# Optimization experiments

Measured on AMD Instinct MI355X. Metric: run time of the kernel, lower is better.

## Reference

```python
import jax, jax.numpy as jnp
import numpy as np

B, N, DIM, HEAD = 4, 2048, 1024, 16
HD = DIM // HEAD
LN_EPS = 1e-5


def setup_inputs() -> dict:
    key = jax.random.key(0)
    k1, k2, k3, k4 = jax.random.split(key, 4)
    x = jax.random.normal(k1, (B, N, DIM), dtype=jnp.float32)
    A = jax.random.normal(k2, (B, N, HEAD, 1), dtype=jnp.float32)
    ln_w = jnp.ones((DIM,), dtype=jnp.float32)
    ln_b = jnp.zeros((DIM,), dtype=jnp.float32)
    Wqk = jax.random.normal(k3, (2 * DIM, DIM), dtype=jnp.float32) * (DIM ** -0.5)
    wv = jax.random.normal(k4, (1, 1), dtype=jnp.float32)
    return {"x": x, "A": A, "ln_w": ln_w, "ln_b": ln_b, "Wqk": Wqk, "wv": wv}


def reference(x, A, ln_w, ln_b, Wqk, wv):
    b, n, dim = x.shape
    head = A.shape[2]
    hd = dim // head
    scale = dim ** -0.5  # NOTE: source uses full-dim scale, not head_dim

    # LayerNorm
    mu = jnp.mean(x, axis=-1, keepdims=True)
    xc = x - mu
    var = jnp.mean(xc * xc, axis=-1, keepdims=True)
    xn = xc * jax.lax.rsqrt(var + LN_EPS) * ln_w + ln_b

    # QK projection: [B,N,2*dim] -> q,k [B,head,N,hd]
    qk = jnp.einsum('bnd,ed->bne', xn, Wqk)
    qk = qk.reshape(b, n, 2, head, hd)
    q = qk[:, :, 0].transpose(0, 2, 1, 3)  # [B,H,N,hd]
    k = qk[:, :, 1].transpose(0, 2, 1, 3)

    # v = Linear(1,1,bias=False)(A), head-major layout [B,H,N,1]
    v = (A * wv[0, 0]).transpose(0, 2, 1, 3)

    scores = jnp.einsum('bhnd,bhmd->bhnm', q, k) * scale  # [B,H,N,N]
    attn = jax.nn.softmax(scores, axis=-1)
    out = jnp.einsum('bhnm,bhme->bhne', attn, v)  # [B,H,N,1]
    A_plus = out.transpose(0, 2, 1, 3)  # [B,N,H,1]
    return A + A_plus
```

## Files before the change

kernel.cpp:

```cpp
#include <hip/hip_runtime.h>

#define B_    4
#define N_    2048
#define DIM_  1024
#define HEAD_ 16
#define HD_   64
#define M_    (B_*N_)
#define E_    (2*DIM_)

typedef short          frag8 __attribute__((ext_vector_type(8)));
typedef float          facc4 __attribute__((ext_vector_type(4)));
typedef unsigned short ush4  __attribute__((ext_vector_type(4)));
typedef _Float16       hv4   __attribute__((ext_vector_type(4)));
typedef _Float16       hv2   __attribute__((ext_vector_type(2)));

#define AS1 __attribute__((address_space(1)))
#define AS3 __attribute__((address_space(3)))

__device__ __forceinline__ void gld_lds16(const void* g, void* l) {
    __builtin_amdgcn_global_load_lds((AS1 void*)(void*)g, (AS3 void*)l, 16, 0, 0);
}

__device__ __forceinline__ unsigned short f2bf(float f) {
    return __builtin_bit_cast(unsigned short, (__bf16)f);
}

__global__ __launch_bounds__(256) void prep_kernel(const float* __restrict__ x,
                                                   const float* __restrict__ lw,
                                                   const float* __restrict__ lb,
                                                   const float* __restrict__ Wqk,
                                                   const float* __restrict__ A,
                                                   const float* __restrict__ wv,
                                                   unsigned short* __restrict__ xn,
                                                   unsigned short* __restrict__ wb,
                                                   unsigned short* __restrict__ v16) {
    __shared__ float red[8];
    const int bid = blockIdx.x;
    const int t   = threadIdx.x;
    if (bid < M_) {
        const float4 v = ((const float4*)(x + (size_t)bid * DIM_))[t];
        float s  = v.x + v.y + v.z + v.w;
        float sq = v.x*v.x + v.y*v.y + v.z*v.z + v.w*v.w;
#pragma unroll
        for (int off = 32; off > 0; off >>= 1) {
            s  += __shfl_xor(s,  off);
            sq += __shfl_xor(sq, off);
        }
        const int w = t >> 6;
        if ((t & 63) == 0) { red[w] = s; red[4 + w] = sq; }
        __syncthreads();
        s  = red[0] + red[1] + red[2] + red[3];
        sq = red[4] + red[5] + red[6] + red[7];
        const float mu   = s * (1.0f / DIM_);
        const float rstd = rsqrtf(sq * (1.0f / DIM_) - mu * mu + 1e-5f);
        const float4 wv4 = ((const float4*)lw)[t];
        const float4 bv4 = ((const float4*)lb)[t];
        ush4 o;
        o[0] = f2bf((v.x - mu) * rstd * wv4.x + bv4.x);
        o[1] = f2bf((v.y - mu) * rstd * wv4.y + bv4.y);
        o[2] = f2bf((v.z - mu) * rstd * wv4.z + bv4.z);
        o[3] = f2bf((v.w - mu) * rstd * wv4.w + bv4.w);
        *(ush4*)(xn + (size_t)bid * DIM_ + t * 4) = o;
    } else if (bid < M_ + 2048) {
        const int i = (bid - M_) * 256 + t;
        const float4 v = ((const float4*)Wqk)[i];
        ush4 o;
        o[0] = f2bf(v.x); o[1] = f2bf(v.y); o[2] = f2bf(v.z); o[3] = f2bf(v.w);
        ((ush4*)wb)[i] = o;
    } else {
        const int bh = bid - (M_ + 2048);
        const int b = bh >> 4, h = bh & 15;
        const float wvv = wv[0];
#pragma unroll
        for (int i = 0; i < 8; ++i) {
            const int n = i * 256 + t;
            const float f = A[((size_t)(b * N_ + n)) * HEAD_ + h] * wvv;
            v16[(size_t)bh * N_ + n] = __builtin_bit_cast(unsigned short, (_Float16)f);
        }
    }
}

__global__ __launch_bounds__(512, 2) void gemm_qk(const unsigned short* __restrict__ xn,
                                                  const unsigned short* __restrict__ wb,
                                                  unsigned short* __restrict__ qo,
                                                  unsigned short* __restrict__ ko) {
    __shared__ __attribute__((aligned(16))) char lds[131072];
    const int t    = threadIdx.x;
    const int lane = t & 63;
    const int wid  = t >> 6;
    const int wr   = wid >> 2, wc = wid & 3;
    const int lr   = lane & 15, lg = lane >> 4;
    const int bid  = blockIdx.x;
    const int bm   = bid & 31, bn = bid >> 5;
    const int m0   = bm * 256, e0 = bn * 256;

    const int srow = t >> 3;
    const int ss8  = ((t & 7) ^ (srow & 7)) * 8;
    const int wu16 = (t & ~63) * 16;

    facc4 acc[8][4] = {};
    frag8 a[4][2], b[2][2];

#define STG(mat, tile, half) do {                                              \
        const unsigned short* sp_ = (mat) ? wb : xn;                           \
        const int rb_ = (mat) ? e0 : m0;                                       \
        _Pragma("unroll")                                                      \
        for (int l_ = 0; l_ < 2; ++l_)                                         \
            gld_lds16(sp_ + (size_t)(rb_ + (half)*128 + l_*64 + srow) * DIM_   \
                          + (tile)*64 + ss8,                                   \
                      lds + ((tile)&1)*65536 + (mat)*32768 + (half)*16384      \
                          + l_*8192 + wu16);                                   \
    } while (0)

#define LDA(mh) do {                                                           \
        _Pragma("unroll")                                                      \
        for (int mf_ = 0; mf_ < 4; ++mf_) {                                    \
            const int row_ = wr*128 + (mh)*64 + mf_*16 + lr;                   \
            const int sw_  = (row_ & 7) << 4;                                  \
            const char* ab_ = lds + cb*65536;                                  \
            a[mf_][0] = *(const frag8*)(ab_ + row_*128 + ((lg*16) ^ sw_));     \
            a[mf_][1] = *(const frag8*)(ab_ + row_*128 + ((64 + lg*16) ^ sw_));\
        }                                                                      \
    } while (0)

#define LDB(nh) do {                                                           \
        _Pragma("unroll")                                                      \
        for (int nf_ = 0; nf_ < 2; ++nf_) {                                    \
            const int row_ = wc*64 + (nh)*32 + nf_*16 + lr;                    \
            const int sw_  = (row_ & 7) << 4;                                  \
            const char* bb_ = lds + cb*65536 + 32768;                          \
            b[nf_][0] = *(const frag8*)(bb_ + row_*128 + ((lg*16) ^ sw_));     \
            b[nf_][1] = *(const frag8*)(bb_ + row_*128 + ((64 + lg*16) ^ sw_));\
        }                                                                      \
    } while (0)

#define MM(mh, nh) do {                                                        \
        __builtin_amdgcn_s_setprio(1);                                         \
        _Pragma("unroll")                                                      \
        for (int mf_ = 0; mf_ < 4; ++mf_)                                      \
        _Pragma("unroll")                                                      \
        for (int nf_ = 0; nf_ < 2; ++nf_) {                                    \
            acc[(mh)*4+mf_][(nh)*2+nf_] = __builtin_amdgcn_mfma_f32_16x16x32_bf16( \
                a[mf_][0], b[nf_][0], acc[(mh)*4+mf_][(nh)*2+nf_], 0, 0, 0);   \
            acc[(mh)*4+mf_][(nh)*2+nf_] = __builtin_amdgcn_mfma_f32_16x16x32_bf16( \
                a[mf_][1], b[nf_][1], acc[(mh)*4+mf_][(nh)*2+nf_], 0, 0, 0);   \
        }                                                                      \
        __builtin_amdgcn_s_setprio(0);                                         \
    } while (0)

#define PH_SYNC(NW) do {                                                       \
        asm volatile("s_waitcnt vmcnt(" NW ")" ::: "memory");                  \
        __builtin_amdgcn_s_barrier();                                          \
        asm volatile("" ::: "memory");                                         \
    } while (0)
#define PH_BAR() do {                                                          \
        __builtin_amdgcn_s_barrier();                                          \
        asm volatile("" ::: "memory");                                         \
    } while (0)
#define PH_LGKM() do {                                                         \
        asm volatile("s_waitcnt lgkmcnt(0)" ::: "memory");                     \
        __builtin_amdgcn_sched_barrier(0);                                     \
    } while (0)

    STG(0, 0, 0);  STG(1, 0, 0);  STG(0, 0, 1);  STG(1, 0, 1);
    STG(0, 1, 0);  STG(0, 1, 1);  STG(1, 1, 0);

    for (int m = 0; m < 15; ++m) {
        const int cb = m & 1;
        PH_SYNC("8");
        LDA(0); LDB(0);
        STG(1, m + 1, 1);
        PH_LGKM();
        MM(0, 0);
        PH_SYNC("8");
        LDB(1);
        if (m <= 13) STG(0, m + 2, 0);
        PH_LGKM();
        MM(0, 1);
        PH_SYNC("8");
        LDA(1); LDB(0);
        PH_LGKM();
        MM(1, 0);
        PH_SYNC("8");
        LDB(1);
        if (m <= 13) { STG(0, m + 2, 1); STG(1, m + 2, 0); }
        PH_LGKM();
        MM(1, 1);
    }
    {
        const int cb = 1;
        PH_SYNC("2");  LDA(0); LDB(0); PH_LGKM(); MM(0, 0);
        PH_SYNC("0");  LDB(1);         PH_LGKM(); MM(0, 1);
        PH_BAR();      LDA(1); LDB(0); PH_LGKM(); MM(1, 0);
        PH_BAR();      LDB(1);         PH_LGKM(); MM(1, 1);
    }
#undef STG
#undef LDA
#undef LDB
#undef MM
#undef PH_SYNC
#undef PH_BAR
#undef PH_LGKM

    const float QSCALE = 0.03125f * 1.4426950408889634f;
#pragma unroll
    for (int mf8 = 0; mf8 < 8; ++mf8) {
#pragma unroll
        for (int nf4 = 0; nf4 < 4; ++nf4) {
            const int eg = e0 + wc * 64 + nf4 * 16 + lr;
#pragma unroll
            for (int r = 0; r < 4; ++r) {
                const int   mg = m0 + wr * 128 + mf8 * 16 + lg * 4 + r;
                const int   b_  = mg >> 11;
                const int   n  = mg & (N_ - 1);
                const float val = acc[mf8][nf4][r];
                if (eg < DIM_) {
                    const int h = eg >> 6, d = eg & 63;
                    qo[((size_t)((b_ * HEAD_ + h) * N_ + n)) * HD_ + d] = f2bf(val * QSCALE);
                } else {
                    const int e2 = eg - DIM_;
                    const int h = e2 >> 6, d = e2 & 63;
                    ko[((size_t)((b_ * HEAD_ + h) * N_ + n)) * HD_ + d] = f2bf(val);
                }
            }
        }
    }
}

__global__ __launch_bounds__(256) void attn_kernel(const unsigned short* __restrict__ q,
                                                   const unsigned short* __restrict__ kmat,
                                                   const unsigned short* __restrict__ v16,
                                                   float2* __restrict__ part) {
    __shared__ __attribute__((aligned(16))) char KsB[3 * 8192];
    const int t    = threadIdx.x;
    const int lane = t & 63, w = t >> 6;
    const int lr   = lane & 15, lg = lane >> 4;
    const int id    = blockIdx.x;
    const int split = id >> 9;
    const int bh    = (id >> 3) & 63;
    const int qblk  = id & 7;
    const int b     = bh >> 4, h = bh & 15;
    const int q0    = qblk * 256 + w * 64;

    const int row0  = t >> 3;
    const int koff  = row0 * HD_ + (((t & 7) ^ (row0 & 7)) * 8);
    const int wbase = (t & ~63) * 16;
    const int sw    = (lr & 7) << 4;
    const int off_h0 = lr * 128 + ((lg * 16) ^ sw);
    const int off_h1 = lr * 128 + ((64 + lg * 16) ^ sw);

    const unsigned short* qbase = q    + (size_t)bh * N_ * HD_;
    const unsigned short* kfix  = kmat + (size_t)bh * N_ * HD_ + (size_t)split * 512 * HD_;
    const unsigned short* vfix  = v16  + (size_t)bh * N_ + split * 512;

    frag8 qf[4][2];
#pragma unroll
    for (int qt = 0; qt < 4; ++qt) {
#pragma unroll
        for (int hh = 0; hh < 2; ++hh)
            qf[qt][hh] = *(const frag8*)(qbase + (size_t)(q0 + qt * 16 + lr) * HD_ + hh * 32 + lg * 8);
    }

    hv4 sel, one1;
#pragma unroll
    for (int j = 0; j < 4; ++j) {
        sel[j]  = (lr == 0) ? (_Float16)1.f : (_Float16)0.f;
        one1[j] = (lr == 1) ? (_Float16)1.f : (_Float16)0.f;
    }
    const facc4 z4 = {0.f, 0.f, 0.f, 0.f};
    facc4 acc[4] = {};

#define STAGE(c) do {                                                          \
        gld_lds16(kfix + (c) * 64 * HD_ + koff,                                \
                  KsB + ((c) % 3) * 8192 + wbase);                             \
        gld_lds16(kfix + (c) * 64 * HD_ + koff + 2048,                         \
                  KsB + ((c) % 3) * 8192 + 4096 + wbase);                      \
    } while (0)

#define CHUNK(c) do {                                                          \
        __builtin_amdgcn_s_setprio(1);                                         \
        _Pragma("unroll")                                                      \
        for (int ct = 0; ct < 4; ++ct) {                                       \
            const frag8 kf0 = *(const frag8*)(KsB + ((c) % 3) * 8192 + ct * 2048 + off_h0); \
            const frag8 kf1 = *(const frag8*)(KsB + ((c) % 3) * 8192 + ct * 2048 + off_h1); \
            const hv4 vv = *(const hv4*)(vfix + (c) * 64 + ct * 16 + lg * 4);  \
            const hv4 av = vv * sel + one1;                                    \
            _Pragma("unroll")                                                  \
            for (int qt = 0; qt < 4; ++qt) {                                   \
                facc4 s_ = __builtin_amdgcn_mfma_f32_16x16x32_bf16(kf0, qf[qt][0], z4, 0, 0, 0); \
                s_ = __builtin_amdgcn_mfma_f32_16x16x32_bf16(kf1, qf[qt][1], s_, 0, 0, 0); \
                const hv2 p01 = __builtin_bit_cast(hv2,                        \
                    __builtin_amdgcn_cvt_pkrtz(__builtin_amdgcn_exp2f(s_[0]),  \
                                               __builtin_amdgcn_exp2f(s_[1]))); \
                const hv2 p23 = __builtin_bit_cast(hv2,                        \
                    __builtin_amdgcn_cvt_pkrtz(__builtin_amdgcn_exp2f(s_[2]),  \
                                               __builtin_amdgcn_exp2f(s_[3]))); \
                hv4 pb; pb[0] = p01[0]; pb[1] = p01[1]; pb[2] = p23[0]; pb[3] = p23[1]; \
                acc[qt] = __builtin_amdgcn_mfma_f32_16x16x16f16(av, pb, acc[qt], 0, 0, 0); \
            }                                                                  \
        }                                                                      \
        __builtin_amdgcn_s_setprio(0);                                         \
    } while (0)

#define ITER_S(c, Nw) {                                                        \
        asm volatile("s_waitcnt vmcnt(" Nw ")" ::: "memory");                  \
        __builtin_amdgcn_s_barrier();                                          \
        asm volatile("" ::: "memory");                                         \
        STAGE((c) + 2);                                                        \
        CHUNK(c);                                                              \
    }
#define ITER_N(c, Nw) {                                                        \
        asm volatile("s_waitcnt vmcnt(" Nw ")" ::: "memory");                  \
        __builtin_amdgcn_s_barrier();                                          \
        asm volatile("" ::: "memory");                                         \
        CHUNK(c);                                                              \
    }

    STAGE(0);
    STAGE(1);
    ITER_S(0, "2") ITER_S(1, "2") ITER_S(2, "2") ITER_S(3, "2")
    ITER_S(4, "2") ITER_S(5, "2") ITER_N(6, "2") ITER_N(7, "0")

#undef STAGE
#undef CHUNK
#undef ITER_S
#undef ITER_N

    if (lg == 0) {
#pragma unroll
        for (int qt = 0; qt < 4; ++qt) {
            const int row = q0 + qt * 16 + lr;
            float2 pr; pr.x = acc[qt][0]; pr.y = acc[qt][1];
            part[(size_t)split * (M_ * HEAD_) + ((size_t)(b * N_ + row)) * HEAD_ + h] = pr;
        }
    }
}

__global__ __launch_bounds__(256) void reduce_kernel(const float2* __restrict__ part,
                                                     const float* __restrict__ Ain,
                                                     float* __restrict__ outp) {
    const int i = blockIdx.x * 256 + threadIdx.x;
    const float2 p0 = part[i];
    const float2 p1 = part[1 * (M_ * HEAD_) + i];
    const float2 p2 = part[2 * (M_ * HEAD_) + i];
    const float2 p3 = part[3 * (M_ * HEAD_) + i];
    outp[i] = Ain[i] + (p0.x + p1.x + p2.x + p3.x) / (p0.y + p1.y + p2.y + p3.y);
}

extern "C" void kernel_launch(void* const* d_in, const int* in_sizes, int n_in,
                              void* d_out, int out_size, void* d_ws, size_t ws_size,
                              hipStream_t stream) {
    const float* x   = (const float*)d_in[0];
    const float* A   = (const float*)d_in[1];
    const float* lw  = (const float*)d_in[2];
    const float* lb  = (const float*)d_in[3];
    const float* Wqk = (const float*)d_in[4];
    const float* wv  = (const float*)d_in[5];
    float* outp = (float*)d_out;

    char* ws = (char*)d_ws;
    unsigned short* xn  = (unsigned short*)(ws);
    unsigned short* wb  = (unsigned short*)(ws + 16u * 1024 * 1024);
    unsigned short* qb  = (unsigned short*)(ws + 20u * 1024 * 1024);
    unsigned short* kb  = (unsigned short*)(ws + 36u * 1024 * 1024);
    unsigned short* v16 = (unsigned short*)(ws + 52u * 1024 * 1024);
    float2*         part = (float2*)(ws);

    prep_kernel<<<M_ + 2048 + B_ * HEAD_, 256, 0, stream>>>(x, lw, lb, Wqk, A, wv, xn, wb, v16);
    gemm_qk<<<256, 512, 0, stream>>>(xn, wb, qb, kb);
    attn_kernel<<<2048, 256, 0, stream>>>(qb, kb, v16, part);
    reduce_kernel<<<(M_ * HEAD_) / 256, 256, 0, stream>>>(part, A, outp);
}
```

Before: 103.0 us.

## Replace PV MFMA with scalar FMA accumulation and double queries per wave

Because the value dimension is 1, the attention kernel no longer packs exp values to fp16 for a second MFMA. It accumulates numerator and denominator directly with FMAs in fp32 and reduces across lane groups with shuffles at the end. V is stored as fp32, and each wave now handles 128 query rows instead of 64, which halves the grid and reuses each staged K chunk across twice as many queries. This removes the pack/convert and extra MFMA work and improves K reuse, at the cost of more VGPRs (16 Q fragments plus accumulators) and fewer blocks in flight.

```diff
diff --git a/kernel.cpp b/kernel.cpp
--- a/kernel.cpp
+++ b/kernel.cpp
@@ -11,8 +11,6 @@
 typedef short          frag8 __attribute__((ext_vector_type(8)));
 typedef float          facc4 __attribute__((ext_vector_type(4)));
 typedef unsigned short ush4  __attribute__((ext_vector_type(4)));
-typedef _Float16       hv4   __attribute__((ext_vector_type(4)));
-typedef _Float16       hv2   __attribute__((ext_vector_type(2)));
 
 #define AS1 __attribute__((address_space(1)))
 #define AS3 __attribute__((address_space(3)))
@@ -33,7 +31,7 @@
                                                    const float* __restrict__ wv,
                                                    unsigned short* __restrict__ xn,
                                                    unsigned short* __restrict__ wb,
-                                                   unsigned short* __restrict__ v16) {
+                                                   float* __restrict__ v32) {
     __shared__ float red[8];
     const int bid = blockIdx.x;
     const int t   = threadIdx.x;
@@ -74,8 +72,7 @@
 #pragma unroll
         for (int i = 0; i < 8; ++i) {
             const int n = i * 256 + t;
-            const float f = A[((size_t)(b * N_ + n)) * HEAD_ + h] * wvv;
-            v16[(size_t)bh * N_ + n] = __builtin_bit_cast(unsigned short, (_Float16)f);
+            v32[(size_t)bh * N_ + n] = A[((size_t)(b * N_ + n)) * HEAD_ + h] * wvv;
         }
     }
 }
@@ -229,18 +226,18 @@
 
 __global__ __launch_bounds__(256) void attn_kernel(const unsigned short* __restrict__ q,
                                                    const unsigned short* __restrict__ kmat,
-                                                   const unsigned short* __restrict__ v16,
+                                                   const float* __restrict__ v32,
                                                    float2* __restrict__ part) {
     __shared__ __attribute__((aligned(16))) char KsB[3 * 8192];
     const int t    = threadIdx.x;
     const int lane = t & 63, w = t >> 6;
     const int lr   = lane & 15, lg = lane >> 4;
     const int id    = blockIdx.x;
-    const int split = id >> 9;
-    const int bh    = (id >> 3) & 63;
-    const int qblk  = id & 7;
+    const int split = id >> 8;
+    const int bh    = (id >> 2) & 63;
+    const int qblk  = id & 3;
     const int b     = bh >> 4, h = bh & 15;
-    const int q0    = qblk * 256 + w * 64;
+    const int q0    = qblk * 512 + w * 128;
 
     const int row0  = t >> 3;
     const int koff  = row0 * HD_ + (((t & 7) ^ (row0 & 7)) * 8);
@@ -251,24 +248,18 @@
 
     const unsigned short* qbase = q    + (size_t)bh * N_ * HD_;
     const unsigned short* kfix  = kmat + (size_t)bh * N_ * HD_ + (size_t)split * 512 * HD_;
-    const unsigned short* vfix  = v16  + (size_t)bh * N_ + split * 512;
-
-    frag8 qf[4][2];
-#pragma unroll
-    for (int qt = 0; qt < 4; ++qt) {
+    const float*          vfix  = v32  + (size_t)bh * N_ + split * 512;
+
+    frag8 qf[8][2];
+#pragma unroll
+    for (int qt = 0; qt < 8; ++qt) {
 #pragma unroll
         for (int hh = 0; hh < 2; ++hh)
             qf[qt][hh] = *(const frag8*)(qbase + (size_t)(q0 + qt * 16 + lr) * HD_ + hh * 32 + lg * 8);
     }
 
-    hv4 sel, one1;
-#pragma unroll
-    for (int j = 0; j < 4; ++j) {
-        sel[j]  = (lr == 0) ? (_Float16)1.f : (_Float16)0.f;
-        one1[j] = (lr == 1) ? (_Float16)1.f : (_Float16)0.f;
-    }
     const facc4 z4 = {0.f, 0.f, 0.f, 0.f};
-    facc4 acc[4] = {};
+    float num[8] = {}, den[8] = {};
 
 #define STAGE(c) do {                                                          \
         gld_lds16(kfix + (c) * 64 * HD_ + koff,                                \
@@ -283,20 +274,20 @@
         for (int ct = 0; ct < 4; ++ct) {                                       \
             const frag8 kf0 = *(const frag8*)(KsB + ((c) % 3) * 8192 + ct * 2048 + off_h0); \
             const frag8 kf1 = *(const frag8*)(KsB + ((c) % 3) * 8192 + ct * 2048 + off_h1); \
-            const hv4 vv = *(const hv4*)(vfix + (c) * 64 + ct * 16 + lg * 4);  \
-            const hv4 av = vv * sel + one1;                                    \
+            const float4 vv = *(const float4*)(vfix + (c) * 64 + ct * 16 + lg * 4); \
             _Pragma("unroll")                                                  \
-            for (int qt = 0; qt < 4; ++qt) {                                   \
+            for (int qt = 0; qt < 8; ++qt) {                                   \
                 facc4 s_ = __builtin_amdgcn_mfma_f32_16x16x32_bf16(kf0, qf[qt][0], z4, 0, 0, 0); \
                 s_ = __builtin_amdgcn_mfma_f32_16x16x32_bf16(kf1, qf[qt][1], s_, 0, 0, 0); \
-                const hv2 p01 = __builtin_bit_cast(hv2,                        \
-                    __builtin_amdgcn_cvt_pkrtz(__builtin_amdgcn_exp2f(s_[0]),  \
-                                               __builtin_amdgcn_exp2f(s_[1]))); \
-                const hv2 p23 = __builtin_bit_cast(hv2,                        \
-                    __builtin_amdgcn_cvt_pkrtz(__builtin_amdgcn_exp2f(s_[2]),  \
-                                               __builtin_amdgcn_exp2f(s_[3]))); \
-                hv4 pb; pb[0] = p01[0]; pb[1] = p01[1]; pb[2] = p23[0]; pb[3] = p23[1]; \
-                acc[qt] = __builtin_amdgcn_mfma_f32_16x16x16f16(av, pb, acc[qt], 0, 0, 0); \
+                const float e0 = __builtin_amdgcn_exp2f(s_[0]);                \
+                const float e1 = __builtin_amdgcn_exp2f(s_[1]);                \
+                const float e2 = __builtin_amdgcn_exp2f(s_[2]);                \
+                const float e3 = __builtin_amdgcn_exp2f(s_[3]);                \
+                den[qt] += (e0 + e1) + (e2 + e3);                              \
+                num[qt] = fmaf(e0, vv.x, num[qt]);                             \
+                num[qt] = fmaf(e1, vv.y, num[qt]);                             \
+                num[qt] = fmaf(e2, vv.z, num[qt]);                             \
+                num[qt] = fmaf(e3, vv.w, num[qt]);                             \
             }                                                                  \
         }                                                                      \
         __builtin_amdgcn_s_setprio(0);                                         \
@@ -326,11 +317,14 @@
 #undef ITER_S
 #undef ITER_N
 
-    if (lg == 0) {
-#pragma unroll
-        for (int qt = 0; qt < 4; ++qt) {
+#pragma unroll
+    for (int qt = 0; qt < 8; ++qt) {
+        float n_ = num[qt], d_ = den[qt];
+        n_ += __shfl_xor(n_, 16); d_ += __shfl_xor(d_, 16);
+        n_ += __shfl_xor(n_, 32); d_ += __shfl_xor(d_, 32);
+        if (lg == 0) {
             const int row = q0 + qt * 16 + lr;
-            float2 pr; pr.x = acc[qt][0]; pr.y = acc[qt][1];
+            float2 pr; pr.x = n_; pr.y = d_;
             part[(size_t)split * (M_ * HEAD_) + ((size_t)(b * N_ + row)) * HEAD_ + h] = pr;
         }
     }
@@ -363,11 +357,11 @@
     unsigned short* wb  = (unsigned short*)(ws + 16u * 1024 * 1024);
     unsigned short* qb  = (unsigned short*)(ws + 20u * 1024 * 1024);
     unsigned short* kb  = (unsigned short*)(ws + 36u * 1024 * 1024);
-    unsigned short* v16 = (unsigned short*)(ws + 52u * 1024 * 1024);
+    float*          v32 = (float*)(ws + 52u * 1024 * 1024);
     float2*         part = (float2*)(ws);
 
-    prep_kernel<<<M_ + 2048 + B_ * HEAD_, 256, 0, stream>>>(x, lw, lb, Wqk, A, wv, xn, wb, v16);
+    prep_kernel<<<M_ + 2048 + B_ * HEAD_, 256, 0, stream>>>(x, lw, lb, Wqk, A, wv, xn, wb, v32);
     gemm_qk<<<256, 512, 0, stream>>>(xn, wb, qb, kb);
-    attn_kernel<<<2048, 256, 0, stream>>>(qb, kb, v16, part);
+    attn_kernel<<<1024, 256, 0, stream>>>(qb, kb, v32, part);
     reduce_kernel<<<(M_ * HEAD_) / 256, 256, 0, stream>>>(part, A, outp);
 }
```

Measured after the change: 292.7 us. +184.1%, slower.
